# Kernel optimization log

Measured on AMD Instinct MI355X. Metric: run time of the kernel, lower is better.

## Reference

```python
import jax, jax.numpy as jnp
import numpy as np
import math

M = 4096   # mem_dim == hidden_size (required: C @ qt)
D = 2048   # input_size


def setup_inputs() -> dict:
    key = jax.random.key(0)
    ks = jax.random.split(key, 16)
    f = lambda k, s: jax.random.normal(k, s, dtype=jnp.float32)
    return {
        "x": f(ks[0], (D, 1)),
        "cp": f(ks[1], (M, M)),
        "n_prev": f(ks[2], (M, 1)),
        "Wq": f(ks[3], (M, D)),
        "bq": f(ks[4], (M, 1)),
        "Wk": f(ks[5], (M, D)),
        "bk": f(ks[6], (M, 1)),
        "Wv": f(ks[7], (M, D)),
        "bV": f(ks[8], (M, 1)),
        "Wi": f(ks[9], (1, D)),
        "bi": f(ks[10], (1,)),
        "Wf": f(ks[11], (1, D)),
        "bf": f(ks[12], (1,)),
        "Wo": f(ks[13], (1, D)),
        "bo": f(ks[14], (1,)),
    }


def reference(x, cp, n_prev, Wq, bq, Wk, bk, Wv, bV, Wi, bi, Wf, bf, Wo, bo):
    inv_sqrt_m = 1.0 / math.sqrt(M)
    qt = Wq @ x + bq                      # (M, 1)
    kt = inv_sqrt_m * (Wk @ x + bk)       # (M, 1)
    vt = Wv @ x + bV                      # (M, 1)
    it = jnp.exp(Wi @ x + bi)             # (1, 1) input gate (exp)
    ft = jnp.exp(Wf @ x + bf)             # (1, 1) forget gate (exp)
    v = vt[:, 0]                          # (M,)
    k = kt[:, 0]                          # (M,)
    # matrix memory update: C = f*C_prev + i * v k^T
    C = ft * cp + it * jnp.outer(v, k)    # (M, M)
    n = ft * n_prev + it * k[:, None]     # (M, 1)
    denom = jnp.maximum(jnp.abs(n.T @ qt), 1.0)   # (1, 1)
    h_tilde = (C @ qt) / denom            # (M, 1)
    ot = jax.nn.sigmoid(Wo @ x + bo)      # (1, 1)
    ht = ot * h_tilde                     # (M, 1)
    return (ht, C, n)
```

## Files before the change

kernel.cpp:

```cpp
#include <hip/hip_runtime.h>
#include <math.h>

#define MM 4096
#define DD 2048


__global__ __launch_bounds__(256) void gemv3_kernel(
    const float* __restrict__ Wq, const float* __restrict__ bq,
    const float* __restrict__ Wk, const float* __restrict__ bk,
    const float* __restrict__ Wv, const float* __restrict__ bV,
    const float* __restrict__ x, float* __restrict__ ws)
{
    int wave  = (blockIdx.x * blockDim.x + threadIdx.x) >> 6;
    int lane  = threadIdx.x & 63;
    int which = wave >> 12;
    int row   = wave & (MM - 1);
    const float* W = (which == 0) ? Wq : ((which == 1) ? Wk : Wv);
    const float* b = (which == 0) ? bq : ((which == 1) ? bk : bV);
    const float4* wrow = (const float4*)(W + (size_t)row * DD);
    const float4* xv   = (const float4*)x;
    float acc = 0.f;
    #pragma unroll
    for (int t = 0; t < DD / 4 / 64; ++t) {
        float4 w  = wrow[lane + 64 * t];
        float4 xx = xv  [lane + 64 * t];
        acc += w.x * xx.x + w.y * xx.y + w.z * xx.z + w.w * xx.w;
    }
    for (int off = 32; off; off >>= 1) acc += __shfl_down(acc, off, 64);
    if (lane == 0) {
        float r = acc + b[row];
        if (which == 1) r *= (1.0f / 64.0f);
        ws[which * MM + row] = r;
    }
}

__global__ __launch_bounds__(256) void scalars_kernel(
    const float* __restrict__ Wi, const float* __restrict__ bi,
    const float* __restrict__ Wf, const float* __restrict__ bf,
    const float* __restrict__ Wo, const float* __restrict__ bo,
    const float* __restrict__ x, float* __restrict__ ws)
{
    __shared__ double sred[3][4];
    double a0 = 0, a1 = 0, a2 = 0;
    const float4* xv  = (const float4*)x;
    const float4* wiv = (const float4*)Wi;
    const float4* wfv = (const float4*)Wf;
    const float4* wov = (const float4*)Wo;
    for (int t = threadIdx.x; t < DD / 4; t += 256) {
        float4 xx = xv[t];
        float4 wi4 = wiv[t];
        a0 += (double)wi4.x * xx.x + (double)wi4.y * xx.y + (double)wi4.z * xx.z + (double)wi4.w * xx.w;
        float4 wf4 = wfv[t];
        a1 += (double)wf4.x * xx.x + (double)wf4.y * xx.y + (double)wf4.z * xx.z + (double)wf4.w * xx.w;
        float4 wo4 = wov[t];
        a2 += (double)wo4.x * xx.x + (double)wo4.y * xx.y + (double)wo4.z * xx.z + (double)wo4.w * xx.w;
    }
    int lane = threadIdx.x & 63, wid = threadIdx.x >> 6;
    for (int off = 32; off; off >>= 1) {
        a0 += __shfl_down(a0, off, 64);
        a1 += __shfl_down(a1, off, 64);
        a2 += __shfl_down(a2, off, 64);
    }
    if (lane == 0) { sred[0][wid] = a0; sred[1][wid] = a1; sred[2][wid] = a2; }
    __syncthreads();
    if (threadIdx.x == 0) {
        double s0 = 0, s1 = 0, s2 = 0;
        for (int w = 0; w < 4; ++w) { s0 += sred[0][w]; s1 += sred[1][w]; s2 += sred[2][w]; }
        ws[3 * MM + 0] = (float)exp(s0 + (double)bi[0]);
        ws[3 * MM + 1] = (float)exp(s1 + (double)bf[0]);
        ws[3 * MM + 2] = (float)(1.0 / (1.0 + exp(-(s2 + (double)bo[0]))));
    }
}

__global__ __launch_bounds__(1024) void n_denom_kernel(
    const float* __restrict__ n_prev, float* __restrict__ ws, float* __restrict__ n_out)
{
    __shared__ float sred[16];
    float it = ws[3 * MM + 0], ft = ws[3 * MM + 1];
    float acc = 0.f;
    for (int i = threadIdx.x; i < MM; i += 1024) {
        float ni = fmaf(ft, n_prev[i], it * ws[MM + i]);
        n_out[i] = ni;
        acc = fmaf(ni, ws[i], acc);
    }
    int lane = threadIdx.x & 63, wid = threadIdx.x >> 6;
    for (int off = 32; off; off >>= 1) acc += __shfl_down(acc, off, 64);
    if (lane == 0) sred[wid] = acc;
    __syncthreads();
    if (threadIdx.x == 0) {
        float s = 0.f;
        for (int w = 0; w < 16; ++w) s += sred[w];
        ws[3 * MM + 3] = fmaxf(fabsf(s), 1.0f);
    }
}

__global__ __launch_bounds__(256) void rowC_kernel(
    const float* __restrict__ cp, const float* __restrict__ ws,
    float* __restrict__ C_out, float* __restrict__ ht_out)
{
    __shared__ float sred[4];
    int row = blockIdx.x;
    float it = ws[3 * MM + 0], ft = ws[3 * MM + 1];
    float ot = ws[3 * MM + 2], denom = ws[3 * MM + 3];
    float ivi = it * ws[2 * MM + row];
    const float4* cprow = (const float4*)(cp + (size_t)row * MM);
    float4*       crow  = (float4*)(C_out + (size_t)row * MM);
    const float4* kv = (const float4*)(ws + MM);
    const float4* qv = (const float4*)ws;
    float acc = 0.f;
    #pragma unroll 4
    for (int t = threadIdx.x; t < MM / 4; t += 256) {
        float4 c = cprow[t], kk = kv[t], qq = qv[t];
        float4 o;
        o.x = fmaf(ivi, kk.x, ft * c.x);
        o.y = fmaf(ivi, kk.y, ft * c.y);
        o.z = fmaf(ivi, kk.z, ft * c.z);
        o.w = fmaf(ivi, kk.w, ft * c.w);
        crow[t] = o;
        acc += o.x * qq.x + o.y * qq.y + o.z * qq.z + o.w * qq.w;
    }
    int lane = threadIdx.x & 63, wid = threadIdx.x >> 6;
    for (int off = 32; off; off >>= 1) acc += __shfl_down(acc, off, 64);
    if (lane == 0) sred[wid] = acc;
    __syncthreads();
    if (threadIdx.x == 0) {
        float s = sred[0] + sred[1] + sred[2] + sred[3];
        ht_out[row] = ot * (s / denom);
    }
}

extern "C" void kernel_launch(void* const* d_in, const int* in_sizes, int n_in,
                              void* d_out, int out_size, void* d_ws, size_t ws_size,
                              hipStream_t stream)
{
    const float* x      = (const float*)d_in[0];
    const float* cp     = (const float*)d_in[1];
    const float* n_prev = (const float*)d_in[2];
    const float* Wq = (const float*)d_in[3];
    const float* bq = (const float*)d_in[4];
    const float* Wk = (const float*)d_in[5];
    const float* bk = (const float*)d_in[6];
    const float* Wv = (const float*)d_in[7];
    const float* bV = (const float*)d_in[8];
    const float* Wi = (const float*)d_in[9];
    const float* bi = (const float*)d_in[10];
    const float* Wf = (const float*)d_in[11];
    const float* bf = (const float*)d_in[12];
    const float* Wo = (const float*)d_in[13];
    const float* bo = (const float*)d_in[14];

    float* out = (float*)d_out;
    float* ht  = out;
    float* C   = out + MM;
    float* n   = out + MM + (size_t)MM * MM;
    float* ws  = (float*)d_ws;

    gemv3_kernel  <<<3 * MM / 4, 256, 0, stream>>>(Wq, bq, Wk, bk, Wv, bV, x, ws);
    scalars_kernel<<<1, 256, 0, stream>>>(Wi, bi, Wf, bf, Wo, bo, x, ws);
    n_denom_kernel<<<1, 1024, 0, stream>>>(n_prev, ws, n);
    rowC_kernel   <<<MM, 256, 0, stream>>>(cp, ws, C, ht);
}
```

Before: 230.1 us.

## Fuse gate scalars into GEMV, fold n/denom into rowC, process four rows per block

Merges the three gate dot-products into the QKV GEMV launch as extra blocks, and each GEMV wave now computes q, k and v for one row with x staged in shared memory. The n update and denom reduction move into block 0 of the C-update kernel. That kernel now handles four rows per block with k and q cached in LDS, and the final h scaling runs in a small third kernel. The goal is fewer launches and serial single-block kernels, plus better reuse of q/k. The cost is one extra kernel and a workspace round-trip for the row sums.

```diff
diff --git a/kernel.cpp b/kernel.cpp
--- a/kernel.cpp
+++ b/kernel.cpp
@@ -5,128 +5,188 @@
 #define DD 2048
 
 
-__global__ __launch_bounds__(256) void gemv3_kernel(
+__global__ __launch_bounds__(256) void k1_gemv_gates(
+    const float* __restrict__ x,
     const float* __restrict__ Wq, const float* __restrict__ bq,
     const float* __restrict__ Wk, const float* __restrict__ bk,
     const float* __restrict__ Wv, const float* __restrict__ bV,
-    const float* __restrict__ x, float* __restrict__ ws)
-{
-    int wave  = (blockIdx.x * blockDim.x + threadIdx.x) >> 6;
-    int lane  = threadIdx.x & 63;
-    int which = wave >> 12;
-    int row   = wave & (MM - 1);
-    const float* W = (which == 0) ? Wq : ((which == 1) ? Wk : Wv);
-    const float* b = (which == 0) ? bq : ((which == 1) ? bk : bV);
-    const float4* wrow = (const float4*)(W + (size_t)row * DD);
-    const float4* xv   = (const float4*)x;
-    float acc = 0.f;
-    #pragma unroll
-    for (int t = 0; t < DD / 4 / 64; ++t) {
-        float4 w  = wrow[lane + 64 * t];
-        float4 xx = xv  [lane + 64 * t];
-        acc += w.x * xx.x + w.y * xx.y + w.z * xx.z + w.w * xx.w;
-    }
-    for (int off = 32; off; off >>= 1) acc += __shfl_down(acc, off, 64);
-    if (lane == 0) {
-        float r = acc + b[row];
-        if (which == 1) r *= (1.0f / 64.0f);
-        ws[which * MM + row] = r;
-    }
-}
-
-__global__ __launch_bounds__(256) void scalars_kernel(
     const float* __restrict__ Wi, const float* __restrict__ bi,
     const float* __restrict__ Wf, const float* __restrict__ bf,
     const float* __restrict__ Wo, const float* __restrict__ bo,
-    const float* __restrict__ x, float* __restrict__ ws)
-{
-    __shared__ double sred[3][4];
-    double a0 = 0, a1 = 0, a2 = 0;
-    const float4* xv  = (const float4*)x;
-    const float4* wiv = (const float4*)Wi;
-    const float4* wfv = (const float4*)Wf;
-    const float4* wov = (const float4*)Wo;
-    for (int t = threadIdx.x; t < DD / 4; t += 256) {
-        float4 xx = xv[t];
-        float4 wi4 = wiv[t];
-        a0 += (double)wi4.x * xx.x + (double)wi4.y * xx.y + (double)wi4.z * xx.z + (double)wi4.w * xx.w;
-        float4 wf4 = wfv[t];
-        a1 += (double)wf4.x * xx.x + (double)wf4.y * xx.y + (double)wf4.z * xx.z + (double)wf4.w * xx.w;
-        float4 wo4 = wov[t];
-        a2 += (double)wo4.x * xx.x + (double)wo4.y * xx.y + (double)wo4.z * xx.z + (double)wo4.w * xx.w;
-    }
-    int lane = threadIdx.x & 63, wid = threadIdx.x >> 6;
+    float* __restrict__ ws)
+{
+    const int lane = threadIdx.x & 63;
+    const int wid  = threadIdx.x >> 6;
+
+    if (blockIdx.x >= 1024) {
+        __shared__ double gred[4];
+        const int g = blockIdx.x - 1024;
+        const float* G = (g == 0) ? Wi : ((g == 1) ? Wf : Wo);
+        const float4* g4 = (const float4*)G;
+        const float4* xv = (const float4*)x;
+        double acc = 0.0;
+        for (int t = threadIdx.x; t < DD / 4; t += 256) {
+            float4 gg = g4[t];
+            float4 xx = xv[t];
+            acc += (double)gg.x * xx.x + (double)gg.y * xx.y
+                 + (double)gg.z * xx.z + (double)gg.w * xx.w;
+        }
+        for (int off = 32; off; off >>= 1) acc += __shfl_down(acc, off, 64);
+        if (lane == 0) gred[wid] = acc;
+        __syncthreads();
+        if (threadIdx.x == 0) {
+            double s = gred[0] + gred[1] + gred[2] + gred[3];
+            if (g == 0)      ws[3 * MM + 0] = (float)exp(s + (double)bi[0]);
+            else if (g == 1) ws[3 * MM + 1] = (float)exp(s + (double)bf[0]);
+            else             ws[3 * MM + 2] = (float)(1.0 / (1.0 + exp(-(s + (double)bo[0]))));
+        }
+        return;
+    }
+
+    __shared__ float xs[DD];
+    {
+        const float4* xv  = (const float4*)x;
+        float4*       xsv = (float4*)xs;
+        xsv[threadIdx.x]       = xv[threadIdx.x];
+        xsv[256 + threadIdx.x] = xv[256 + threadIdx.x];
+    }
+    __syncthreads();
+
+    const int row = blockIdx.x * 4 + wid;
+    const float4* wq = (const float4*)(Wq + (size_t)row * DD);
+    const float4* wk = (const float4*)(Wk + (size_t)row * DD);
+    const float4* wv = (const float4*)(Wv + (size_t)row * DD);
+
+    float4 rq[8], rk[8], rv[8];
+    #pragma unroll
+    for (int t = 0; t < 8; ++t) rq[t] = wq[lane + 64 * t];
+    #pragma unroll
+    for (int t = 0; t < 8; ++t) rk[t] = wk[lane + 64 * t];
+    #pragma unroll
+    for (int t = 0; t < 8; ++t) rv[t] = wv[lane + 64 * t];
+
+    const float4* xs4 = (const float4*)xs;
+    float aq = 0.f, ak = 0.f, av = 0.f;
+    #pragma unroll
+    for (int t = 0; t < 8; ++t) {
+        float4 xx = xs4[lane + 64 * t];
+        aq += rq[t].x * xx.x + rq[t].y * xx.y + rq[t].z * xx.z + rq[t].w * xx.w;
+        ak += rk[t].x * xx.x + rk[t].y * xx.y + rk[t].z * xx.z + rk[t].w * xx.w;
+        av += rv[t].x * xx.x + rv[t].y * xx.y + rv[t].z * xx.z + rv[t].w * xx.w;
+    }
     for (int off = 32; off; off >>= 1) {
-        a0 += __shfl_down(a0, off, 64);
-        a1 += __shfl_down(a1, off, 64);
-        a2 += __shfl_down(a2, off, 64);
-    }
-    if (lane == 0) { sred[0][wid] = a0; sred[1][wid] = a1; sred[2][wid] = a2; }
-    __syncthreads();
-    if (threadIdx.x == 0) {
-        double s0 = 0, s1 = 0, s2 = 0;
-        for (int w = 0; w < 4; ++w) { s0 += sred[0][w]; s1 += sred[1][w]; s2 += sred[2][w]; }
-        ws[3 * MM + 0] = (float)exp(s0 + (double)bi[0]);
-        ws[3 * MM + 1] = (float)exp(s1 + (double)bf[0]);
-        ws[3 * MM + 2] = (float)(1.0 / (1.0 + exp(-(s2 + (double)bo[0]))));
-    }
-}
-
-__global__ __launch_bounds__(1024) void n_denom_kernel(
-    const float* __restrict__ n_prev, float* __restrict__ ws, float* __restrict__ n_out)
-{
+        aq += __shfl_down(aq, off, 64);
+        ak += __shfl_down(ak, off, 64);
+        av += __shfl_down(av, off, 64);
+    }
+    if (lane == 0) {
+        ws[row]          = aq + bq[row];
+        ws[MM + row]     = (ak + bk[row]) * (1.0f / 64.0f);
+        ws[2 * MM + row] = av + bV[row];
+    }
+}
+
+__global__ __launch_bounds__(256) void k2_rowC(
+    const float* __restrict__ cp, const float* __restrict__ n_prev,
+    float* __restrict__ ws, float* __restrict__ C_out, float* __restrict__ n_out)
+{
+    __shared__ float ks[MM];
+    __shared__ float qs[MM];
     __shared__ float sred[16];
-    float it = ws[3 * MM + 0], ft = ws[3 * MM + 1];
-    float acc = 0.f;
-    for (int i = threadIdx.x; i < MM; i += 1024) {
-        float ni = fmaf(ft, n_prev[i], it * ws[MM + i]);
-        n_out[i] = ni;
-        acc = fmaf(ni, ws[i], acc);
-    }
-    int lane = threadIdx.x & 63, wid = threadIdx.x >> 6;
-    for (int off = 32; off; off >>= 1) acc += __shfl_down(acc, off, 64);
-    if (lane == 0) sred[wid] = acc;
-    __syncthreads();
-    if (threadIdx.x == 0) {
-        float s = 0.f;
-        for (int w = 0; w < 16; ++w) s += sred[w];
-        ws[3 * MM + 3] = fmaxf(fabsf(s), 1.0f);
-    }
-}
-
-__global__ __launch_bounds__(256) void rowC_kernel(
-    const float* __restrict__ cp, const float* __restrict__ ws,
-    float* __restrict__ C_out, float* __restrict__ ht_out)
-{
-    __shared__ float sred[4];
-    int row = blockIdx.x;
-    float it = ws[3 * MM + 0], ft = ws[3 * MM + 1];
-    float ot = ws[3 * MM + 2], denom = ws[3 * MM + 3];
-    float ivi = it * ws[2 * MM + row];
-    const float4* cprow = (const float4*)(cp + (size_t)row * MM);
-    float4*       crow  = (float4*)(C_out + (size_t)row * MM);
-    const float4* kv = (const float4*)(ws + MM);
-    const float4* qv = (const float4*)ws;
-    float acc = 0.f;
-    #pragma unroll 4
-    for (int t = threadIdx.x; t < MM / 4; t += 256) {
-        float4 c = cprow[t], kk = kv[t], qq = qv[t];
-        float4 o;
-        o.x = fmaf(ivi, kk.x, ft * c.x);
-        o.y = fmaf(ivi, kk.y, ft * c.y);
-        o.z = fmaf(ivi, kk.z, ft * c.z);
-        o.w = fmaf(ivi, kk.w, ft * c.w);
-        crow[t] = o;
-        acc += o.x * qq.x + o.y * qq.y + o.z * qq.z + o.w * qq.w;
-    }
-    int lane = threadIdx.x & 63, wid = threadIdx.x >> 6;
-    for (int off = 32; off; off >>= 1) acc += __shfl_down(acc, off, 64);
-    if (lane == 0) sred[wid] = acc;
-    __syncthreads();
-    if (threadIdx.x == 0) {
-        float s = sred[0] + sred[1] + sred[2] + sred[3];
-        ht_out[row] = ot * (s / denom);
-    }
+    const int lane = threadIdx.x & 63;
+    const int wid  = threadIdx.x >> 6;
+
+    const float it = ws[3 * MM + 0];
+    const float ft = ws[3 * MM + 1];
+
+    if (blockIdx.x == 0) {
+        const float4* np4 = (const float4*)n_prev;
+        const float4* kv4 = (const float4*)(ws + MM);
+        const float4* qv4 = (const float4*)ws;
+        float4* n4 = (float4*)n_out;
+        float acc = 0.f;
+        #pragma unroll
+        for (int j = 0; j < MM / 4 / 256; ++j) {
+            int t = threadIdx.x + 256 * j;
+            float4 np = np4[t], kk = kv4[t], qq = qv4[t];
+            float4 nn;
+            nn.x = fmaf(ft, np.x, it * kk.x);
+            nn.y = fmaf(ft, np.y, it * kk.y);
+            nn.z = fmaf(ft, np.z, it * kk.z);
+            nn.w = fmaf(ft, np.w, it * kk.w);
+            n4[t] = nn;
+            acc += nn.x * qq.x + nn.y * qq.y + nn.z * qq.z + nn.w * qq.w;
+        }
+        for (int off = 32; off; off >>= 1) acc += __shfl_down(acc, off, 64);
+        if (lane == 0) sred[wid] = acc;
+        __syncthreads();
+        if (threadIdx.x == 0) {
+            float s = sred[0] + sred[1] + sred[2] + sred[3];
+            ws[3 * MM + 3] = fmaxf(fabsf(s), 1.0f);
+        }
+        __syncthreads();
+    }
+
+    {
+        const float4* kv4 = (const float4*)(ws + MM);
+        const float4* qv4 = (const float4*)ws;
+        float4* ks4 = (float4*)ks;
+        float4* qs4 = (float4*)qs;
+        #pragma unroll
+        for (int j = 0; j < MM / 4 / 256; ++j) {
+            int t = threadIdx.x + 256 * j;
+            ks4[t] = kv4[t];
+            qs4[t] = qv4[t];
+        }
+    }
+    __syncthreads();
+
+    const float4* ks4 = (const float4*)ks;
+    const float4* qs4 = (const float4*)qs;
+    float rowacc[4];
+    #pragma unroll
+    for (int j = 0; j < 4; ++j) {
+        const int row = blockIdx.x * 4 + j;
+        const float ivi = it * ws[2 * MM + row];
+        const float4* cprow = (const float4*)(cp + (size_t)row * MM);
+        float4*       crow  = (float4*)(C_out + (size_t)row * MM);
+        float acc = 0.f;
+        #pragma unroll
+        for (int u = 0; u < MM / 4 / 256; ++u) {
+            int t = threadIdx.x + 256 * u;
+            float4 c = cprow[t], kk = ks4[t], qq = qs4[t];
+            float4 o;
+            o.x = fmaf(ivi, kk.x, ft * c.x);
+            o.y = fmaf(ivi, kk.y, ft * c.y);
+            o.z = fmaf(ivi, kk.z, ft * c.z);
+            o.w = fmaf(ivi, kk.w, ft * c.w);
+            crow[t] = o;
+            acc += o.x * qq.x + o.y * qq.y + o.z * qq.z + o.w * qq.w;
+        }
+        rowacc[j] = acc;
+    }
+    __syncthreads();
+    #pragma unroll
+    for (int j = 0; j < 4; ++j) {
+        float acc = rowacc[j];
+        for (int off = 32; off; off >>= 1) acc += __shfl_down(acc, off, 64);
+        if (lane == 0) sred[j * 4 + wid] = acc;
+    }
+    __syncthreads();
+    if (threadIdx.x < 4) {
+        int j = threadIdx.x;
+        float s = sred[j * 4 + 0] + sred[j * 4 + 1] + sred[j * 4 + 2] + sred[j * 4 + 3];
+        ws[4 * MM + blockIdx.x * 4 + j] = s;
+    }
+}
+
+__global__ __launch_bounds__(256) void k3_finalize(
+    const float* __restrict__ ws, float* __restrict__ ht_out)
+{
+    const float ot    = ws[3 * MM + 2];
+    const float denom = ws[3 * MM + 3];
+    const int i = blockIdx.x * 256 + threadIdx.x;
+    ht_out[i] = ot * (ws[4 * MM + i] / denom);
 }
 
 extern "C" void kernel_launch(void* const* d_in, const int* in_sizes, int n_in,
@@ -155,8 +215,8 @@
     float* n   = out + MM + (size_t)MM * MM;
     float* ws  = (float*)d_ws;
 
-    gemv3_kernel  <<<3 * MM / 4, 256, 0, stream>>>(Wq, bq, Wk, bk, Wv, bV, x, ws);
-    scalars_kernel<<<1, 256, 0, stream>>>(Wi, bi, Wf, bf, Wo, bo, x, ws);
-    n_denom_kernel<<<1, 1024, 0, stream>>>(n_prev, ws, n);
-    rowC_kernel   <<<MM, 256, 0, stream>>>(cp, ws, C, ht);
-}
+    k1_gemv_gates<<<1027, 256, 0, stream>>>(x, Wq, bq, Wk, bk, Wv, bV,
+                                            Wi, bi, Wf, bf, Wo, bo, ws);
+    k2_rowC      <<<1024, 256, 0, stream>>>(cp, n_prev, ws, C, n);
+    k3_finalize  <<<MM / 256, 256, 0, stream>>>(ws, ht);
+}
```

Result: no change. 232.0 us (+0.8%).
